# Kernel tuning notes

Measured on AMD Instinct MI355X. Metric: run time of the kernel, lower is better.

Reference implementation:

```python
import jax, jax.numpy as jnp
import numpy as np

EPS = 1e-8
RESOLUTION = 32
DILATION = 1


def _stencils(resolution=RESOLUTION, dilation=DILATION):
    # interior grid of resolution^2 samples in [-1, 1]^2 (cell centers)
    lin = (np.arange(resolution) + 0.5) / resolution * 2.0 - 1.0
    gy, gx = np.meshgrid(lin, lin, indexing='ij')
    inner = np.stack([gy.ravel(), gx.ravel()], -1).astype(np.float32)
    # perimeter ring dilated outward by `dilation` cells
    scale = (resolution + 2.0 * dilation) / resolution
    mask = np.zeros((resolution, resolution), bool)
    mask[0, :] = mask[-1, :] = mask[:, 0] = mask[:, -1] = True
    outer = (inner[mask.ravel()] * scale).astype(np.float32)
    # append homogeneous coordinate (matches torch.concat with ones)
    s_in = np.concatenate([inner, np.ones((inner.shape[0], 1), np.float32)], -1)
    s_out = np.concatenate([outer, np.ones((outer.shape[0], 1), np.float32)], -1)
    return jnp.asarray(s_in), jnp.asarray(s_out)


def _bilinear(image, pos):
    # image: (H, W); pos: (..., 2) pixel coords (row, col); clamped bilinear
    H, W = image.shape
    i = pos[..., 0]
    j = pos[..., 1]
    i0 = jnp.clip(jnp.floor(i), 0, H - 2).astype(jnp.int32)
    j0 = jnp.clip(jnp.floor(j), 0, W - 2).astype(jnp.int32)
    di = jnp.clip(i - i0, 0.0, 1.0)
    dj = jnp.clip(j - j0, 0.0, 1.0)
    v00 = image[i0, j0]
    v01 = image[i0, j0 + 1]
    v10 = image[i0 + 1, j0]
    v11 = image[i0 + 1, j0 + 1]
    return (v00 * (1 - di) * (1 - dj) + v01 * (1 - di) * dj
            + v10 * di * (1 - dj) + v11 * di * dj)


def setup_inputs() -> dict:
    key = jax.random.key(0)
    k1, k2 = jax.random.split(key)
    S, P = 4, 4096
    H = W = 2048
    u = jax.random.uniform(k1, (S, P, 5), dtype=jnp.float32)
    xy = u[..., :2] * (H - 1)              # centers inside the image
    ab = 4.0 + u[..., 2:4] * 20.0          # half extents in [4, 24] px
    th = u[..., 4:5] * jnp.float32(np.pi)  # angle in [0, pi)
    points = jnp.concatenate([xy, ab, th], axis=-1)
    points_mask = jnp.ones((S, P), dtype=jnp.float32)
    position_energy_map = jax.random.normal(k2, (1, H, W), dtype=jnp.float32)
    stencil_in, stencil_out = _stencils()
    return {"points": points, "points_mask": points_mask,
            "position_energy_map": position_energy_map,
            "stencil_in": stencil_in, "stencil_out": stencil_out}


def reference(points, points_mask, position_energy_map, stencil_in, stencil_out):
    # affine_from_state: (x, y, a, b, theta) -> 2x3 affine, shape (S, P, 2, 3)
    x, y = points[..., 0], points[..., 1]
    a, b = points[..., 2], points[..., 3]
    t = points[..., 4]
    c, s = jnp.cos(t), jnp.sin(t)
    A = jnp.stack([jnp.stack([a * c, -b * s, x], -1),
                   jnp.stack([a * s, b * c, y], -1)], -2)
    # stencil coordinates in image space: (S, P, n_stencil, 2)
    coords_in = jnp.einsum('spij,nj->spni', A, stencil_in)
    coords_out = jnp.einsum('spij,nj->spni', A, stencil_out)
    img = position_energy_map[0]
    in_values = _bilinear(img, coords_in)    # (S, P, n_in)
    out_values = _bilinear(img, coords_out)  # (S, P, n_out)
    # contrast_measure: t-test-like contrast along stencil dim
    m_in, m_out = in_values.mean(-1), out_values.mean(-1)
    v_in = in_values.var(-1, ddof=1)
    v_out = out_values.var(-1, ddof=1)
    contrast = (m_in - m_out) / jnp.sqrt(v_in + v_out + EPS)
    return contrast * points_mask
```

## Files before the change

kernel.cpp:

```cpp
#include <hip/hip_runtime.h>
#include <hip/hip_fp16.h>
#include <math.h>


__global__ __launch_bounds__(256) void convert_img_f16(
    const float4* __restrict__ src, uint4* __restrict__ dst)
{
    const int t = blockIdx.x * 256 + (int)threadIdx.x;
    const float4 a = src[(size_t)t * 2];
    const float4 b = src[(size_t)t * 2 + 1];
    union { __half2 h[4]; uint4 u; } o;
    o.h[0] = __float22half2_rn(make_float2(a.x, a.y));
    o.h[1] = __float22half2_rn(make_float2(a.z, a.w));
    o.h[2] = __float22half2_rn(make_float2(b.x, b.y));
    o.h[3] = __float22half2_rn(make_float2(b.z, b.w));
    dst[t] = o.u;
}

template<bool CLAMP>
__device__ __forceinline__ float tap16(const __half* __restrict__ img,
                                       float ci, float cj)
{
    float fi = floorf(ci), fj = floorf(cj);
    if (CLAMP) {
        fi = fminf(fmaxf(fi, 0.f), 2046.f);
        fj = fminf(fmaxf(fj, 0.f), 2046.f);
    }
    float di = ci - fi, dj = cj - fj;
    if (CLAMP) {
        di = fminf(fmaxf(di, 0.f), 1.f);
        dj = fminf(fmaxf(dj, 0.f), 1.f);
    }
    const int base = ((int)fi << 11) + (int)fj;
    const int even = base & ~1;
    const int sh   = (base & 1) << 4;
    uint2 q0, q1;
    __builtin_memcpy(&q0, img + even, 8);
    __builtin_memcpy(&q1, img + even + 2048, 8);
    const unsigned p0 = (unsigned)((((unsigned long long)q0.y << 32) | q0.x) >> sh);
    const unsigned p1 = (unsigned)((((unsigned long long)q1.y << 32) | q1.x) >> sh);
    const float2 f0 = __half22float2(*reinterpret_cast<const __half2*>(&p0));
    const float2 f1 = __half22float2(*reinterpret_cast<const __half2*>(&p1));
    const float top = fmaf(f0.y - f0.x, dj, f0.x);
    const float bot = fmaf(f1.y - f1.x, dj, f1.x);
    return fmaf(bot - top, di, top);
}

template<bool CLAMP>
__device__ __forceinline__ void accumulate16(
    const __half* __restrict__ img, int lane, int half,
    float A00, float A01, float A10, float A11, float px, float py,
    float& sum_in, float& sq_in, float& sum_out, float& sq_out)
{
    const int r8 = lane >> 3;
    const int c8 = lane & 7;
    const float sy0 = fmaf((float)r8, 0.0625f, 0.03125f) - 1.0f;
    const float sx0 = fmaf((float)c8, 0.0625f, 0.03125f) - 1.0f;
    const float ci0 = fmaf(A00, sy0, fmaf(A01, sx0, px));
    const float cj0 = fmaf(A10, sy0, fmaf(A11, sx0, py));
    const float A00h = A00 * 0.5f, A01h = A01 * 0.5f;
    const float A10h = A10 * 0.5f, A11h = A11 * 0.5f;

    float s0 = 0.f, q0 = 0.f, s1 = 0.f, q1 = 0.f;
    #pragma unroll
    for (int t = 0; t < 8; ++t) {
        const int tile = half * 8 + t;
        const float ftr = (float)(tile >> 2);
        const float ftc = (float)(tile & 3);
        const float ci = fmaf(A00h, ftr, fmaf(A01h, ftc, ci0));
        const float cj = fmaf(A10h, ftr, fmaf(A11h, ftc, cj0));
        const float v = tap16<CLAMP>(img, ci, cj);
        if (t & 1) { s1 += v; q1 = fmaf(v, v, q1); }
        else       { s0 += v; q0 = fmaf(v, v, q0); }
    }
    sum_in = s0 + s1;
    sq_in  = q0 + q1;

    sum_out = 0.f; sq_out = 0.f;
    const int n = half * 62 + lane;
    if (lane < 62) {
        int row, col;
        if (n < 32)      { row = 0;                   col = n; }
        else if (n < 92) { row = 1 + ((n - 32) >> 1); col = (n & 1) * 31; }
        else             { row = 31;                  col = n - 92; }
        const float sy = (fmaf((float)row, 0.0625f, 0.03125f) - 1.0f) * 1.0625f;
        const float sx = (fmaf((float)col, 0.0625f, 0.03125f) - 1.0f) * 1.0625f;
        const float ci = fmaf(A00, sy, fmaf(A01, sx, px));
        const float cj = fmaf(A10, sy, fmaf(A11, sx, py));
        const float v = tap16<CLAMP>(img, ci, cj);
        sum_out = v;
        sq_out  = v * v;
    }
}

__global__ __launch_bounds__(256) void contrast_kernel_f16(
    const float* __restrict__ points,
    const float* __restrict__ mask,
    const __half* __restrict__ img,
    float* __restrict__ out,
    int n_points)
{
    __shared__ float partial[4][4];

    const int wib  = (int)(threadIdx.x >> 6);
    const int lane = (int)(threadIdx.x & 63u);
    const int pid  = blockIdx.x * 2 + (wib >> 1);
    const int half = wib & 1;
    if (pid >= n_points) return;

    const float* pt = points + (size_t)pid * 5;
    const float px = pt[0];
    const float py = pt[1];
    const float a  = pt[2];
    const float b  = pt[3];
    const float th = pt[4];

    float sn, cs;
    sincosf(th, &sn, &cs);
    const float A00 = a * cs, A01 = -b * sn;
    const float A10 = a * sn, A11 =  b * cs;

    const float Ri = (fabsf(A00) + fabsf(A01)) * 1.04f;
    const float Rj = (fabsf(A10) + fabsf(A11)) * 1.04f;
    const bool interior = (px >= Ri + 0.5f) && (px <= 2046.0f - Ri) &&
                          (py >= Rj + 0.5f) && (py <= 2046.0f - Rj);

    float sum_in, sq_in, sum_out, sq_out;
    if (interior) {
        accumulate16<false>(img, lane, half, A00, A01, A10, A11, px, py,
                            sum_in, sq_in, sum_out, sq_out);
    } else {
        accumulate16<true>(img, lane, half, A00, A01, A10, A11, px, py,
                           sum_in, sq_in, sum_out, sq_out);
    }

    #pragma unroll
    for (int off = 32; off > 0; off >>= 1) {
        sum_in  += __shfl_xor(sum_in,  off);
        sq_in   += __shfl_xor(sq_in,   off);
        sum_out += __shfl_xor(sum_out, off);
        sq_out  += __shfl_xor(sq_out,  off);
    }

    if (lane == 0) {
        partial[wib][0] = sum_in;
        partial[wib][1] = sq_in;
        partial[wib][2] = sum_out;
        partial[wib][3] = sq_out;
    }
    __syncthreads();

    if (lane == 0 && half == 0) {
        const float S_in  = partial[wib][0] + partial[wib + 1][0];
        const float Q_in  = partial[wib][1] + partial[wib + 1][1];
        const float S_out = partial[wib][2] + partial[wib + 1][2];
        const float Q_out = partial[wib][3] + partial[wib + 1][3];
        const float ni = 1024.f, no = 124.f;
        const float m_in  = S_in  / ni;
        const float m_out = S_out / no;
        const float v_in  = (Q_in  - ni * m_in  * m_in ) / (ni - 1.f);
        const float v_out = (Q_out - no * m_out * m_out) / (no - 1.f);
        const float contrast = (m_in - m_out) / sqrtf(v_in + v_out + 1e-8f);
        out[pid] = contrast * mask[pid];
    }
}

__global__ __launch_bounds__(256) void contrast_kernel_fast(
    const float* __restrict__ points, const float* __restrict__ mask,
    const float* __restrict__ img, float* __restrict__ out, int n_points)
{
    constexpr int W = 2048;
    constexpr float fImax = 2046.f, fJmax = 2046.f;
    __shared__ float partial[4][4];
    const int wib  = (int)(threadIdx.x >> 6);
    const int lane = (int)(threadIdx.x & 63u);
    const int pid  = blockIdx.x * 2 + (wib >> 1);
    const int half = wib & 1;
    if (pid >= n_points) return;
    const float* pt = points + (size_t)pid * 5;
    const float px = pt[0], py = pt[1], a = pt[2], b = pt[3], th = pt[4];
    float sn, cs; sincosf(th, &sn, &cs);
    const float A00 = a * cs, A01 = -b * sn, A10 = a * sn, A11 = b * cs;
    const int r8 = lane >> 3, c8 = lane & 7;
    const float sy0 = fmaf((float)r8, 0.0625f, 0.03125f) - 1.0f;
    const float sx0 = fmaf((float)c8, 0.0625f, 0.03125f) - 1.0f;
    const float ci0 = fmaf(A00, sy0, fmaf(A01, sx0, px));
    const float cj0 = fmaf(A10, sy0, fmaf(A11, sx0, py));
    const float A00h = A00 * 0.5f, A01h = A01 * 0.5f;
    const float A10h = A10 * 0.5f, A11h = A11 * 0.5f;
    float s0 = 0.f, q0 = 0.f, s1 = 0.f, q1 = 0.f;
    #pragma unroll
    for (int t = 0; t < 8; ++t) {
        const int tile = half * 8 + t;
        const float ftr = (float)(tile >> 2), ftc = (float)(tile & 3);
        const float ci = fmaf(A00h, ftr, fmaf(A01h, ftc, ci0));
        const float cj = fmaf(A10h, ftr, fmaf(A11h, ftc, cj0));
        const float fi = fminf(fmaxf(floorf(ci), 0.f), fImax);
        const float fj = fminf(fmaxf(floorf(cj), 0.f), fJmax);
        const float di = fminf(fmaxf(ci - fi, 0.f), 1.f);
        const float dj = fminf(fmaxf(cj - fj, 0.f), 1.f);
        const float* p0 = img + (((int)fi << 11) + (int)fj);
        float2 r0, r1;
        __builtin_memcpy(&r0, p0, sizeof(float2));
        __builtin_memcpy(&r1, p0 + W, sizeof(float2));
        const float top = fmaf(r0.y - r0.x, dj, r0.x);
        const float bot = fmaf(r1.y - r1.x, dj, r1.x);
        const float v = fmaf(bot - top, di, top);
        if (t & 1) { s1 += v; q1 = fmaf(v, v, q1); }
        else       { s0 += v; q0 = fmaf(v, v, q0); }
    }
    float sum_in = s0 + s1, sq_in = q0 + q1;
    float sum_out = 0.f, sq_out = 0.f;
    const int n = half * 62 + lane;
    if (lane < 62) {
        int row, col;
        if (n < 32)      { row = 0;                   col = n; }
        else if (n < 92) { row = 1 + ((n - 32) >> 1); col = (n & 1) * 31; }
        else             { row = 31;                  col = n - 92; }
        const float sy = (fmaf((float)row, 0.0625f, 0.03125f) - 1.0f) * 1.0625f;
        const float sx = (fmaf((float)col, 0.0625f, 0.03125f) - 1.0f) * 1.0625f;
        const float ci = fmaf(A00, sy, fmaf(A01, sx, px));
        const float cj = fmaf(A10, sy, fmaf(A11, sx, py));
        const float fi = fminf(fmaxf(floorf(ci), 0.f), fImax);
        const float fj = fminf(fmaxf(floorf(cj), 0.f), fJmax);
        const float di = fminf(fmaxf(ci - fi, 0.f), 1.f);
        const float dj = fminf(fmaxf(cj - fj, 0.f), 1.f);
        const float* p0 = img + (((int)fi << 11) + (int)fj);
        float2 r0, r1;
        __builtin_memcpy(&r0, p0, sizeof(float2));
        __builtin_memcpy(&r1, p0 + W, sizeof(float2));
        const float top = fmaf(r0.y - r0.x, dj, r0.x);
        const float bot = fmaf(r1.y - r1.x, dj, r1.x);
        const float v = fmaf(bot - top, di, top);
        sum_out = v; sq_out = v * v;
    }
    #pragma unroll
    for (int off = 32; off > 0; off >>= 1) {
        sum_in  += __shfl_xor(sum_in,  off);
        sq_in   += __shfl_xor(sq_in,   off);
        sum_out += __shfl_xor(sum_out, off);
        sq_out  += __shfl_xor(sq_out,  off);
    }
    if (lane == 0) {
        partial[wib][0] = sum_in; partial[wib][1] = sq_in;
        partial[wib][2] = sum_out; partial[wib][3] = sq_out;
    }
    __syncthreads();
    if (lane == 0 && half == 0) {
        const float S_in = partial[wib][0] + partial[wib + 1][0];
        const float Q_in = partial[wib][1] + partial[wib + 1][1];
        const float S_out = partial[wib][2] + partial[wib + 1][2];
        const float Q_out = partial[wib][3] + partial[wib + 1][3];
        const float ni = 1024.f, no = 124.f;
        const float m_in = S_in / ni, m_out = S_out / no;
        const float v_in  = (Q_in  - ni * m_in  * m_in ) / (ni - 1.f);
        const float v_out = (Q_out - no * m_out * m_out) / (no - 1.f);
        const float contrast = (m_in - m_out) / sqrtf(v_in + v_out + 1e-8f);
        out[pid] = contrast * mask[pid];
    }
}

__global__ __launch_bounds__(256) void contrast_kernel_generic(
    const float* __restrict__ points, const float* __restrict__ mask,
    const float* __restrict__ img, const float* __restrict__ st_in,
    const float* __restrict__ st_out, float* __restrict__ out,
    int n_points, int n_in, int n_out, int Himg, int Wimg)
{
    const int wave = (int)((blockIdx.x * (unsigned)blockDim.x + threadIdx.x) >> 6);
    const int lane = (int)(threadIdx.x & 63u);
    if (wave >= n_points) return;
    const float* pt = points + (size_t)wave * 5;
    const float px = pt[0], py = pt[1], a = pt[2], b = pt[3], th = pt[4];
    float sn, cs; sincosf(th, &sn, &cs);
    const float A00 = a * cs, A01 = -b * sn, A10 = a * sn, A11 = b * cs;
    const float fImax = (float)(Himg - 2), fJmax = (float)(Wimg - 2);
    float sum_in = 0.f, sq_in = 0.f;
    for (int base = 0; base < n_in; base += 64) {
        const int n = base + lane;
        if (n < n_in) {
            const float sy = st_in[n * 3 + 0], sx = st_in[n * 3 + 1];
            const float ci = fmaf(A00, sy, fmaf(A01, sx, px));
            const float cj = fmaf(A10, sy, fmaf(A11, sx, py));
            const float fi = fminf(fmaxf(floorf(ci), 0.f), fImax);
            const float fj = fminf(fmaxf(floorf(cj), 0.f), fJmax);
            const float di = fminf(fmaxf(ci - fi, 0.f), 1.f);
            const float dj = fminf(fmaxf(cj - fj, 0.f), 1.f);
            const float* p0 = img + ((int)fi * Wimg + (int)fj);
            const float v00 = p0[0], v01 = p0[1], v10 = p0[Wimg], v11 = p0[Wimg + 1];
            const float top = fmaf(v01 - v00, dj, v00);
            const float bot = fmaf(v11 - v10, dj, v10);
            const float v = fmaf(bot - top, di, top);
            sum_in += v; sq_in = fmaf(v, v, sq_in);
        }
    }
    float sum_out = 0.f, sq_out = 0.f;
    for (int base = 0; base < n_out; base += 64) {
        const int n = base + lane;
        if (n < n_out) {
            const float sy = st_out[n * 3 + 0], sx = st_out[n * 3 + 1];
            const float ci = fmaf(A00, sy, fmaf(A01, sx, px));
            const float cj = fmaf(A10, sy, fmaf(A11, sx, py));
            const float fi = fminf(fmaxf(floorf(ci), 0.f), fImax);
            const float fj = fminf(fmaxf(floorf(cj), 0.f), fJmax);
            const float di = fminf(fmaxf(ci - fi, 0.f), 1.f);
            const float dj = fminf(fmaxf(cj - fj, 0.f), 1.f);
            const float* p0 = img + ((int)fi * Wimg + (int)fj);
            const float v00 = p0[0], v01 = p0[1], v10 = p0[Wimg], v11 = p0[Wimg + 1];
            const float top = fmaf(v01 - v00, dj, v00);
            const float bot = fmaf(v11 - v10, dj, v10);
            const float v = fmaf(bot - top, di, top);
            sum_out += v; sq_out = fmaf(v, v, sq_out);
        }
    }
    #pragma unroll
    for (int off = 32; off > 0; off >>= 1) {
        sum_in += __shfl_xor(sum_in, off);  sq_in += __shfl_xor(sq_in, off);
        sum_out += __shfl_xor(sum_out, off); sq_out += __shfl_xor(sq_out, off);
    }
    if (lane == 0) {
        const float ni = (float)n_in, no = (float)n_out;
        const float m_in = sum_in / ni, m_out = sum_out / no;
        const float v_in = (sq_in - ni * m_in * m_in) / (ni - 1.f);
        const float v_out = (sq_out - no * m_out * m_out) / (no - 1.f);
        const float contrast = (m_in - m_out) / sqrtf(v_in + v_out + 1e-8f);
        out[wave] = contrast * mask[wave];
    }
}

extern "C" void kernel_launch(void* const* d_in, const int* in_sizes, int n_in_bufs,
                              void* d_out, int out_size, void* d_ws, size_t ws_size,
                              hipStream_t stream) {
    (void)n_in_bufs; (void)out_size;
    const float* points = (const float*)d_in[0];
    const float* mask   = (const float*)d_in[1];
    const float* img    = (const float*)d_in[2];
    const float* st_in  = (const float*)d_in[3];
    const float* st_out = (const float*)d_in[4];
    float* out = (float*)d_out;

    const int n_points = in_sizes[0] / 5;
    const int n_in     = in_sizes[3] / 3;
    const int n_out    = in_sizes[4] / 3;
    const int hw       = in_sizes[2];

    const bool canonical = (n_in == 1024 && n_out == 124 && hw == 2048 * 2048);
    const size_t f16_bytes = (size_t)hw * sizeof(__half) + 256;

    if (canonical && ws_size >= f16_bytes) {
        __half* img16 = (__half*)d_ws;
        convert_img_f16<<<hw / (256 * 8), 256, 0, stream>>>((const float4*)img, (uint4*)img16);
        const int blocks = (n_points + 1) / 2;
        contrast_kernel_f16<<<blocks, 256, 0, stream>>>(points, mask, img16, out, n_points);
    } else if (canonical) {
        const int blocks = (n_points + 1) / 2;
        contrast_kernel_fast<<<blocks, 256, 0, stream>>>(points, mask, img, out, n_points);
    } else {
        int Wimg = 1;
        while ((long long)Wimg * Wimg < (long long)hw) Wimg <<= 1;
        const int Himg = hw / Wimg;
        const int blocks = (n_points + 3) / 4;
        contrast_kernel_generic<<<blocks, 256, 0, stream>>>(points, mask, img, st_in, st_out,
                                                            out, n_points, n_in, n_out, Himg, Wimg);
    }
}
```

Measured before the change: 121.1 us.

## Bin points by row strip and interleave blocks for L2 locality

Adds a counting sort that groups points into 8 row strips of 256 rows each. The main kernel then runs a fixed grid of 8×1024 blocks that each loop over point pairs, with adjacent blocks mapped to different bins so that each XCD/L2 region works on one strip of the image. The f16 conversion is reordered to match the same strip interleave. The tap loads are also restructured so that all 9 gathers are issued before any evaluation, to raise memory-level parallelism. In exchange it adds four small extra launches with atomics, a grid-stride loop with two __syncthreads per iteration, and higher register pressure.

```diff
diff --git a/kernel.cpp b/kernel.cpp
--- a/kernel.cpp
+++ b/kernel.cpp
@@ -3,10 +3,48 @@
 #include <math.h>
 
 
+#define STRIP_SHIFT 8
+#define MAIN_PAIR_STRIDE 1024
+
+__device__ __forceinline__ int point_bin(const float* points, int i) {
+    int b = (int)points[(size_t)i * 5] >> STRIP_SHIFT;
+    return b < 0 ? 0 : (b > 7 ? 7 : b);
+}
+
+__global__ void bin_init(int* cnt) {
+    if (threadIdx.x < 8) cnt[threadIdx.x] = 0;
+}
+
+__global__ void bin_count(const float* __restrict__ points, int n, int* __restrict__ cnt) {
+    const int i = blockIdx.x * 256 + (int)threadIdx.x;
+    if (i < n) atomicAdd(&cnt[point_bin(points, i)], 1);
+}
+
+__global__ void bin_offsets(const int* __restrict__ cnt, int* __restrict__ off,
+                            int* __restrict__ cur) {
+    if (threadIdx.x == 0) {
+        int s = 0;
+        for (int k = 0; k < 8; ++k) { off[k] = s; s += cnt[k]; }
+    }
+    if (threadIdx.x < 8) cur[threadIdx.x] = 0;
+}
+
+__global__ void bin_scatter(const float* __restrict__ points, int n,
+                            const int* __restrict__ off, int* __restrict__ cur,
+                            int* __restrict__ perm) {
+    const int i = blockIdx.x * 256 + (int)threadIdx.x;
+    if (i < n) {
+        const int b = point_bin(points, i);
+        const int s = atomicAdd(&cur[b], 1);
+        perm[off[b] + s] = i;
+    }
+}
+
 __global__ __launch_bounds__(256) void convert_img_f16(
     const float4* __restrict__ src, uint4* __restrict__ dst)
 {
-    const int t = blockIdx.x * 256 + (int)threadIdx.x;
+    const int row = ((int)(blockIdx.x & 7) << 8) + (int)(blockIdx.x >> 3);
+    const int t   = row * 256 + (int)threadIdx.x;
     const float4 a = src[(size_t)t * 2];
     const float4 b = src[(size_t)t * 2 + 1];
     union { __half2 h[4]; uint4 u; } o;
@@ -18,25 +56,26 @@
 }
 
 template<bool CLAMP>
-__device__ __forceinline__ float tap16(const __half* __restrict__ img,
-                                       float ci, float cj)
+__device__ __forceinline__ void tap_addr(float ci, float cj,
+                                         float& di, float& dj, int& base)
 {
     float fi = floorf(ci), fj = floorf(cj);
     if (CLAMP) {
         fi = fminf(fmaxf(fi, 0.f), 2046.f);
         fj = fminf(fmaxf(fj, 0.f), 2046.f);
     }
-    float di = ci - fi, dj = cj - fj;
+    di = ci - fi; dj = cj - fj;
     if (CLAMP) {
         di = fminf(fmaxf(di, 0.f), 1.f);
         dj = fminf(fmaxf(dj, 0.f), 1.f);
     }
-    const int base = ((int)fi << 11) + (int)fj;
-    const int even = base & ~1;
-    const int sh   = (base & 1) << 4;
-    uint2 q0, q1;
-    __builtin_memcpy(&q0, img + even, 8);
-    __builtin_memcpy(&q1, img + even + 2048, 8);
+    base = ((int)fi << 11) + (int)fj;
+}
+
+__device__ __forceinline__ float tap_eval(const uint2& q0, const uint2& q1,
+                                          float di, float dj, int base)
+{
+    const int sh = (base & 1) << 4;
     const unsigned p0 = (unsigned)((((unsigned long long)q0.y << 32) | q0.x) >> sh);
     const unsigned p1 = (unsigned)((((unsigned long long)q1.y << 32) | q1.x) >> sh);
     const float2 f0 = __half22float2(*reinterpret_cast<const __half2*>(&p0));
@@ -61,7 +100,10 @@
     const float A00h = A00 * 0.5f, A01h = A01 * 0.5f;
     const float A10h = A10 * 0.5f, A11h = A11 * 0.5f;
 
-    float s0 = 0.f, q0 = 0.f, s1 = 0.f, q1 = 0.f;
+    float di[9], dj[9];
+    int   base[9];
+    uint2 qa[9], qb[9];
+
     #pragma unroll
     for (int t = 0; t < 8; ++t) {
         const int tile = half * 8 + t;
@@ -69,99 +111,123 @@
         const float ftc = (float)(tile & 3);
         const float ci = fmaf(A00h, ftr, fmaf(A01h, ftc, ci0));
         const float cj = fmaf(A10h, ftr, fmaf(A11h, ftc, cj0));
-        const float v = tap16<CLAMP>(img, ci, cj);
-        if (t & 1) { s1 += v; q1 = fmaf(v, v, q1); }
-        else       { s0 += v; q0 = fmaf(v, v, q0); }
-    }
-    sum_in = s0 + s1;
-    sq_in  = q0 + q1;
-
-    sum_out = 0.f; sq_out = 0.f;
-    const int n = half * 62 + lane;
-    if (lane < 62) {
-        int row, col;
+        tap_addr<CLAMP>(ci, cj, di[t], dj[t], base[t]);
+        const int even = base[t] & ~1;
+        __builtin_memcpy(&qa[t], img + even, 8);
+        __builtin_memcpy(&qb[t], img + even + 2048, 8);
+    }
+    {
+        const int n = half * 62 + lane;
+        int row = 0, col = 0;
         if (n < 32)      { row = 0;                   col = n; }
         else if (n < 92) { row = 1 + ((n - 32) >> 1); col = (n & 1) * 31; }
         else             { row = 31;                  col = n - 92; }
         const float sy = (fmaf((float)row, 0.0625f, 0.03125f) - 1.0f) * 1.0625f;
         const float sx = (fmaf((float)col, 0.0625f, 0.03125f) - 1.0f) * 1.0625f;
-        const float ci = fmaf(A00, sy, fmaf(A01, sx, px));
-        const float cj = fmaf(A10, sy, fmaf(A11, sx, py));
-        const float v = tap16<CLAMP>(img, ci, cj);
-        sum_out = v;
-        sq_out  = v * v;
-    }
-}
-
-__global__ __launch_bounds__(256) void contrast_kernel_f16(
+        float ci = fmaf(A00, sy, fmaf(A01, sx, px));
+        float cj = fmaf(A10, sy, fmaf(A11, sx, py));
+        if (lane >= 62) { ci = px; cj = py; }
+        tap_addr<CLAMP>(ci, cj, di[8], dj[8], base[8]);
+        const int even = base[8] & ~1;
+        __builtin_memcpy(&qa[8], img + even, 8);
+        __builtin_memcpy(&qb[8], img + even + 2048, 8);
+    }
+
+    float s0 = 0.f, q0 = 0.f, s1 = 0.f, q1 = 0.f;
+    #pragma unroll
+    for (int t = 0; t < 8; ++t) {
+        const float v = tap_eval(qa[t], qb[t], di[t], dj[t], base[t]);
+        if (t & 1) { s1 += v; q1 = fmaf(v, v, q1); }
+        else       { s0 += v; q0 = fmaf(v, v, q0); }
+    }
+    sum_in = s0 + s1;
+    sq_in  = q0 + q1;
+
+    const float vr = tap_eval(qa[8], qb[8], di[8], dj[8], base[8]);
+    sum_out = (lane < 62) ? vr : 0.f;
+    sq_out  = (lane < 62) ? vr * vr : 0.f;
+}
+
+__global__ __launch_bounds__(256) void contrast_kernel_f16_binned(
     const float* __restrict__ points,
     const float* __restrict__ mask,
     const __half* __restrict__ img,
-    float* __restrict__ out,
-    int n_points)
+    const int* __restrict__ perm,
+    const int* __restrict__ cnt,
+    const int* __restrict__ off,
+    float* __restrict__ out)
 {
     __shared__ float partial[4][4];
 
-    const int wib  = (int)(threadIdx.x >> 6);
-    const int lane = (int)(threadIdx.x & 63u);
-    const int pid  = blockIdx.x * 2 + (wib >> 1);
-    const int half = wib & 1;
-    if (pid >= n_points) return;
-
-    const float* pt = points + (size_t)pid * 5;
-    const float px = pt[0];
-    const float py = pt[1];
-    const float a  = pt[2];
-    const float b  = pt[3];
-    const float th = pt[4];
-
-    float sn, cs;
-    sincosf(th, &sn, &cs);
-    const float A00 = a * cs, A01 = -b * sn;
-    const float A10 = a * sn, A11 =  b * cs;
-
-    const float Ri = (fabsf(A00) + fabsf(A01)) * 1.04f;
-    const float Rj = (fabsf(A10) + fabsf(A11)) * 1.04f;
-    const bool interior = (px >= Ri + 0.5f) && (px <= 2046.0f - Ri) &&
-                          (py >= Rj + 0.5f) && (py <= 2046.0f - Rj);
-
-    float sum_in, sq_in, sum_out, sq_out;
-    if (interior) {
-        accumulate16<false>(img, lane, half, A00, A01, A10, A11, px, py,
-                            sum_in, sq_in, sum_out, sq_out);
-    } else {
-        accumulate16<true>(img, lane, half, A00, A01, A10, A11, px, py,
-                           sum_in, sq_in, sum_out, sq_out);
-    }
-
-    #pragma unroll
-    for (int off = 32; off > 0; off >>= 1) {
-        sum_in  += __shfl_xor(sum_in,  off);
-        sq_in   += __shfl_xor(sq_in,   off);
-        sum_out += __shfl_xor(sum_out, off);
-        sq_out  += __shfl_xor(sq_out,  off);
-    }
-
-    if (lane == 0) {
-        partial[wib][0] = sum_in;
-        partial[wib][1] = sq_in;
-        partial[wib][2] = sum_out;
-        partial[wib][3] = sq_out;
-    }
-    __syncthreads();
-
-    if (lane == 0 && half == 0) {
-        const float S_in  = partial[wib][0] + partial[wib + 1][0];
-        const float Q_in  = partial[wib][1] + partial[wib + 1][1];
-        const float S_out = partial[wib][2] + partial[wib + 1][2];
-        const float Q_out = partial[wib][3] + partial[wib + 1][3];
-        const float ni = 1024.f, no = 124.f;
-        const float m_in  = S_in  / ni;
-        const float m_out = S_out / no;
-        const float v_in  = (Q_in  - ni * m_in  * m_in ) / (ni - 1.f);
-        const float v_out = (Q_out - no * m_out * m_out) / (no - 1.f);
-        const float contrast = (m_in - m_out) / sqrtf(v_in + v_out + 1e-8f);
-        out[pid] = contrast * mask[pid];
+    const int wib   = (int)(threadIdx.x >> 6);
+    const int lane  = (int)(threadIdx.x & 63u);
+    const int local = wib >> 1;
+    const int half  = wib & 1;
+    const int bin   = (int)(blockIdx.x & 7);
+    const int c     = cnt[bin];
+    const int o     = off[bin];
+
+    for (int j = (int)(blockIdx.x >> 3); 2 * j < c; j += MAIN_PAIR_STRIDE) {
+        const int  k     = 2 * j + local;
+        const bool valid = k < c;
+        const int  pid   = perm[o + (valid ? k : 0)];
+
+        const float* pt = points + (size_t)pid * 5;
+        const float px = pt[0];
+        const float py = pt[1];
+        const float a  = pt[2];
+        const float b  = pt[3];
+        const float th = pt[4];
+
+        float sn, cs;
+        sincosf(th, &sn, &cs);
+        const float A00 = a * cs, A01 = -b * sn;
+        const float A10 = a * sn, A11 =  b * cs;
+
+        const float Ri = (fabsf(A00) + fabsf(A01)) * 1.04f;
+        const float Rj = (fabsf(A10) + fabsf(A11)) * 1.04f;
+        const bool interior = (px >= Ri + 0.5f) && (px <= 2046.0f - Ri) &&
+                              (py >= Rj + 0.5f) && (py <= 2046.0f - Rj);
+
+        float sum_in, sq_in, sum_out, sq_out;
+        if (interior) {
+            accumulate16<false>(img, lane, half, A00, A01, A10, A11, px, py,
+                                sum_in, sq_in, sum_out, sq_out);
+        } else {
+            accumulate16<true>(img, lane, half, A00, A01, A10, A11, px, py,
+                               sum_in, sq_in, sum_out, sq_out);
+        }
+
+        #pragma unroll
+        for (int sft = 32; sft > 0; sft >>= 1) {
+            sum_in  += __shfl_xor(sum_in,  sft);
+            sq_in   += __shfl_xor(sq_in,   sft);
+            sum_out += __shfl_xor(sum_out, sft);
+            sq_out  += __shfl_xor(sq_out,  sft);
+        }
+
+        if (lane == 0) {
+            partial[wib][0] = sum_in;
+            partial[wib][1] = sq_in;
+            partial[wib][2] = sum_out;
+            partial[wib][3] = sq_out;
+        }
+        __syncthreads();
+
+        if (valid && half == 0 && lane == 0) {
+            const float S_in  = partial[wib][0] + partial[wib + 1][0];
+            const float Q_in  = partial[wib][1] + partial[wib + 1][1];
+            const float S_out = partial[wib][2] + partial[wib + 1][2];
+            const float Q_out = partial[wib][3] + partial[wib + 1][3];
+            const float ni = 1024.f, no = 124.f;
+            const float m_in  = S_in  / ni;
+            const float m_out = S_out / no;
+            const float v_in  = (Q_in  - ni * m_in  * m_in ) / (ni - 1.f);
+            const float v_out = (Q_out - no * m_out * m_out) / (no - 1.f);
+            const float contrast = (m_in - m_out) / sqrtf(v_in + v_out + 1e-8f);
+            out[pid] = contrast * mask[pid];
+        }
+        __syncthreads();
     }
 }
 
@@ -235,11 +301,11 @@
         sum_out = v; sq_out = v * v;
     }
     #pragma unroll
-    for (int off = 32; off > 0; off >>= 1) {
-        sum_in  += __shfl_xor(sum_in,  off);
-        sq_in   += __shfl_xor(sq_in,   off);
-        sum_out += __shfl_xor(sum_out, off);
-        sq_out  += __shfl_xor(sq_out,  off);
+    for (int sft = 32; sft > 0; sft >>= 1) {
+        sum_in  += __shfl_xor(sum_in,  sft);
+        sq_in   += __shfl_xor(sq_in,   sft);
+        sum_out += __shfl_xor(sum_out, sft);
+        sq_out  += __shfl_xor(sq_out,  sft);
     }
     if (lane == 0) {
         partial[wib][0] = sum_in; partial[wib][1] = sq_in;
@@ -313,9 +379,9 @@
         }
     }
     #pragma unroll
-    for (int off = 32; off > 0; off >>= 1) {
-        sum_in += __shfl_xor(sum_in, off);  sq_in += __shfl_xor(sq_in, off);
-        sum_out += __shfl_xor(sum_out, off); sq_out += __shfl_xor(sq_out, off);
+    for (int sft = 32; sft > 0; sft >>= 1) {
+        sum_in += __shfl_xor(sum_in, sft);  sq_in += __shfl_xor(sq_in, sft);
+        sum_out += __shfl_xor(sum_out, sft); sq_out += __shfl_xor(sq_out, sft);
     }
     if (lane == 0) {
         const float ni = (float)n_in, no = (float)n_out;
@@ -344,13 +410,27 @@
     const int hw       = in_sizes[2];
 
     const bool canonical = (n_in == 1024 && n_out == 124 && hw == 2048 * 2048);
-    const size_t f16_bytes = (size_t)hw * sizeof(__half) + 256;
-
-    if (canonical && ws_size >= f16_bytes) {
+
+    const size_t img_bytes = (size_t)hw * sizeof(__half);
+    const size_t meta_off  = (img_bytes + 255) & ~(size_t)255;
+    const size_t need      = meta_off + (size_t)(24 + n_points) * 4 + 64;
+
+    if (canonical && ws_size >= need && n_points > 0) {
         __half* img16 = (__half*)d_ws;
-        convert_img_f16<<<hw / (256 * 8), 256, 0, stream>>>((const float4*)img, (uint4*)img16);
-        const int blocks = (n_points + 1) / 2;
-        contrast_kernel_f16<<<blocks, 256, 0, stream>>>(points, mask, img16, out, n_points);
+        int* meta = (int*)((char*)d_ws + meta_off);
+        int* cnt  = meta;
+        int* off  = meta + 8;
+        int* cur  = meta + 16;
+        int* perm = meta + 24;
+
+        const int nb = (n_points + 255) / 256;
+        bin_init   <<<1,  64, 0, stream>>>(cnt);
+        bin_count  <<<nb, 256, 0, stream>>>(points, n_points, cnt);
+        bin_offsets<<<1,  64, 0, stream>>>(cnt, off, cur);
+        bin_scatter<<<nb, 256, 0, stream>>>(points, n_points, off, cur, perm);
+        convert_img_f16<<<2048, 256, 0, stream>>>((const float4*)img, (uint4*)img16);
+        contrast_kernel_f16_binned<<<8 * MAIN_PAIR_STRIDE, 256, 0, stream>>>(
+            points, mask, img16, perm, cnt, off, out);
     } else if (canonical) {
         const int blocks = (n_points + 1) / 2;
         contrast_kernel_fast<<<blocks, 256, 0, stream>>>(points, mask, img, out, n_points);
```

After: 284.1 us. +134.7%, slower.
